# Kernel optimization log

Measured on AMD Instinct MI355X. Metric: run time of the kernel, lower is better.

The kernel has to match this reference:

```python
import jax, jax.numpy as jnp
import numpy as np

H = 128
K = 20
N = 100000
B = 65536
TIME_SCALE = 1.0
NEG = -1e9


def setup_inputs() -> dict:
    key = jax.random.key(0)
    ks = jax.random.split(key, 16)
    s = 0.05
    return {
        "edge_index": jax.random.randint(ks[0], (2, B), 0, N),
        "edge_timestamp": jax.random.randint(ks[1], (B,), 0, 1000000),
        "hist_neighbors": jax.random.randint(ks[2], (N, K), 0, N),
        "hist_times": jax.random.randint(ks[3], (N, K), 0, 1000000),
        "hist_signs": jax.random.randint(ks[4], (N, K), 0, 2),
        "node_emb": jax.random.normal(ks[5], (N, H), jnp.float32) * s,
        "sign_emb": jax.random.normal(ks[6], (2, H), jnp.float32) * s,
        "tp_w1": jax.random.normal(ks[7], (H,), jnp.float32) * s,   # Linear(1,H) weight (flattened)
        "tp_b1": jax.random.normal(ks[8], (H,), jnp.float32) * s,
        "tp_w2": jax.random.normal(ks[9], (H, H), jnp.float32) * s,  # stored [in,out]
        "tp_b2": jax.random.normal(ks[10], (H,), jnp.float32) * s,
        "em_w1": jax.random.normal(ks[11], (4 * H, H), jnp.float32) * s,
        "em_b1": jax.random.normal(ks[12], (H,), jnp.float32) * s,
        "em_w2": jax.random.normal(ks[13], (H, 1), jnp.float32) * s,
        "em_b2": jax.random.normal(ks[14], (1,), jnp.float32) * s,
    }


def _encode(node_ids, query_times, hist_neighbors, hist_times, hist_signs,
            node_emb, sign_emb, tp_w1, tp_b1, tp_w2, tp_b2):
    # node_ids, query_times: [B]
    neigh = hist_neighbors[node_ids]   # [B,K]
    times = hist_times[node_ids]       # [B,K]
    signs = hist_signs[node_ids]       # [B,K]
    valid = (neigh != -1) & (times < query_times[:, None])
    neigh_c = jnp.where(neigh == -1, 0, neigh)
    neigh_e = node_emb[neigh_c]        # [B,K,H]
    sign_e = sign_emb[signs]           # [B,K,H]
    delta = (query_times[:, None].astype(jnp.float32) - times.astype(jnp.float32)) / TIME_SCALE
    h = jax.nn.relu(delta[..., None] * tp_w1 + tp_b1)           # [B,K,H]
    time_e = jnp.einsum('bkh,hd->bkd', h, tp_w2) + tp_b2        # [B,K,H]
    keys = neigh_e + sign_e + time_e
    query = node_emb[node_ids][:, None]                          # [B,1,H]
    scores = jnp.sum(query * keys, axis=-1) / jnp.sqrt(jnp.float32(H))
    scores = jnp.where(valid, scores, NEG)
    attn = jax.nn.softmax(scores, axis=1)                        # [B,K]
    return jnp.einsum('bk,bkh->bh', attn, keys)                  # [B,H]


def reference(edge_index, edge_timestamp, hist_neighbors, hist_times, hist_signs,
              node_emb, sign_emb, tp_w1, tp_b1, tp_w2, tp_b2,
              em_w1, em_b1, em_w2, em_b2):
    u, v = edge_index[0], edge_index[1]
    zu = _encode(u, edge_timestamp, hist_neighbors, hist_times, hist_signs,
                 node_emb, sign_emb, tp_w1, tp_b1, tp_w2, tp_b2)
    zv = _encode(v, edge_timestamp, hist_neighbors, hist_times, hist_signs,
                 node_emb, sign_emb, tp_w1, tp_b1, tp_w2, tp_b2)
    feat = jnp.concatenate([zu, zv, jnp.abs(zu - zv), zu * zv], axis=1)  # [B,4H]
    hid = jax.nn.relu(feat @ em_w1 + em_b1)
    logits = (hid @ em_w2 + em_b2).squeeze(-1)                           # [B]
    return logits
```

## Files before the change

### kernel.cpp

```cpp
#include <hip/hip_runtime.h>
#include <hip/hip_bf16.h>
#include <math.h>

#define H 128
#define K 20
#define EPB 16

#define WS_TBL    0
#define WS_THM    65792
#define WS_CNT    66176
#define WSB_HI    67072
#define WSB_LO    99840

typedef __attribute__((ext_vector_type(8))) short short8;
typedef __attribute__((ext_vector_type(4))) float f32x4;

template<int CTRL, int RMASK>
__device__ __forceinline__ float dpp_add(float x) {
  int y = __builtin_amdgcn_update_dpp(0, __float_as_int(x), CTRL, RMASK, 0xf, true);
  return x + __int_as_float(y);
}
__device__ __forceinline__ float wave_sum63(float x) {
  x = dpp_add<0xB1,  0xf>(x);
  x = dpp_add<0x4E,  0xf>(x);
  x = dpp_add<0x141, 0xf>(x);
  x = dpp_add<0x140, 0xf>(x);
  x = dpp_add<0x142, 0xa>(x);
  x = dpp_add<0x143, 0xc>(x);
  return x;
}
__device__ __forceinline__ float bcast63(float x) {
  return __int_as_float(__builtin_amdgcn_readlane(__float_as_int(x), 63));
}

__device__ __forceinline__ unsigned short bfbits(float x) {
  __hip_bfloat16 h = __float2bfloat16(x);
  unsigned short u; __builtin_memcpy(&u, &h, 2); return u;
}
__device__ __forceinline__ float bf2f(unsigned short u) {
  return __uint_as_float(((unsigned)u) << 16);
}

__global__ __launch_bounds__(128) void aux_kernel(
    const float* __restrict__ w1v, const float* __restrict__ b1v,
    const float* __restrict__ w2, const float* __restrict__ b2,
    const float* __restrict__ em_w1, float* __restrict__ ws)
{
  int blk = blockIdx.x;
  int tid = threadIdx.x;
  if (blk < 257) {
    __shared__ float th[H];
    __shared__ int grp[H];
    __shared__ int sidx[2 * H];
    __shared__ int Msh;
    float w = w1v[tid], b = b1v[tid];
    int g = (w > 0.f) ? 0 : ((w < 0.f) ? 1 : 2);
    float t = (g == 2) ? 0.f : (-b / w);
    th[tid] = t; grp[tid] = g;
    if (tid == 0) Msh = 0;
    __syncthreads();
    if (g != 2) {
      int r = 0;
      for (int i = 0; i < H; i++)
        if (grp[i] != 2 && (th[i] < t || (th[i] == t && i < tid))) r++;
      sidx[r] = (tid << 1) | (g == 0 ? 1 : 0);
      atomicAdd(&Msh, 1);
      if (blk == 0) ws[WS_THM + r] = t;
    }
    __syncthreads();
    int M = Msh;
    if (blk == 0 && tid == 0) ((int*)(ws + WS_CNT))[0] = M;
    int r = blk;
    if (r > M) return;
    int d = tid;
    float accW = 0.f, accB = b2[d];
    for (int i = 0; i < H; i++)
      if (grp[i] == 2 && b1v[i] > 0.f) accB += b1v[i] * w2[i * H + d];
    #pragma unroll 4
    for (int i = 0; i < M; i++) {
      int ent = sidx[i];
      int h = ent >> 1;
      int isP = ent & 1;
      int take = (i < r) ? isP : (1 - isP);
      if (take) {
        float wv = w2[h * H + d];
        accW += w1v[h] * wv;
        accB += b1v[h] * wv;
      }
    }
    ws[WS_TBL + r * 256 + 2 * d + 0] = accW;
    ws[WS_TBL + r * 256 + 2 * d + 1] = accB;
  } else {
    int idx = (blk - 257) * 128 + tid;
    int j  = idx & 7;
    int l  = (idx >> 3) & 63;
    int kc = (idx >> 9) & 15;
    int c  = idx >> 13;
    int k = kc * 32 + ((l >> 4) * 8) + j;
    int n = c * 16 + (l & 15);
    float x = em_w1[k * H + n];
    unsigned short hb = bfbits(x);
    unsigned short lb = bfbits(x - bf2f(hb));
    ((unsigned short*)(ws + WSB_HI))[idx] = hb;
    ((unsigned short*)(ws + WSB_LO))[idx] = lb;
  }
}

template<int NB>
__device__ __forceinline__ void run_sides(
    int sbase, int b0, int B, int lane,
    const int* __restrict__ edge_index, const int* __restrict__ edge_ts,
    const int* __restrict__ hist_nb, const int* __restrict__ hist_tm,
    const int* __restrict__ hist_sg,
    const float* __restrict__ node_emb, const float* __restrict__ ws,
    float th0, float th1, float th2, float th3,
    float2 se0, float2 se1, float* __restrict__ zbuf)
{
  const float S = 0.088388347648318447f;
  int eBase = sbase >> 1;
  int eN = b0 + eBase;
  int nU = edge_index[eN];
  int nV = edge_index[B + eN];
  int t_n = edge_ts[eN];
  float2 qU_n = *(const float2*)(node_emb + (size_t)nU * H + 2 * lane);
  float2 qV_n = *(const float2*)(node_emb + (size_t)nV * H + 2 * lane);
  int pkU_n = 0, tmU_n = 0, pkV_n = 0, tmV_n = 0;
  if (lane < K) {
    pkU_n = (hist_nb[nU * K + lane] << 1) | hist_sg[nU * K + lane];
    tmU_n = hist_tm[nU * K + lane];
    pkV_n = (hist_nb[nV * K + lane] << 1) | hist_sg[nV * K + lane];
    tmV_n = hist_tm[nV * K + lane];
  }

  #pragma unroll 1
  for (int p = 0; p < 4; p++) {
    int e = eBase + p;
    int tC = t_n;
    float2 qU = qU_n, qV = qV_n;
    int pkU = pkU_n, tmU = tmU_n, pkV = pkV_n, tmV = tmV_n;
    if (p < 3) {
      int e2 = b0 + e + 1;
      int nU2 = edge_index[e2];
      int nV2 = edge_index[B + e2];
      t_n = edge_ts[e2];
      qU_n = *(const float2*)(node_emb + (size_t)nU2 * H + 2 * lane);
      qV_n = *(const float2*)(node_emb + (size_t)nV2 * H + 2 * lane);
      if (lane < K) {
        pkU_n = (hist_nb[nU2 * K + lane] << 1) | hist_sg[nU2 * K + lane];
        tmU_n = hist_tm[nU2 * K + lane];
        pkV_n = (hist_nb[nV2 * K + lane] << 1) | hist_sg[nV2 * K + lane];
        tmV_n = hist_tm[nV2 * K + lane];
      }
    }

    unsigned long long mU0 = __ballot((lane < K) && (tmU < tC) && (pkU >= 0));
    unsigned long long mV0 = __ballot((lane < K) && (tmV < tC) && (pkV >= 0));
    bool fU = (mU0 == 0), fV = (mV0 == 0);
    unsigned long long mU = fU ? 0xFFFFFull : mU0;
    unsigned long long mV = fV ? 0xFFFFFull : mV0;
    float qUx = qU.x * S, qUy = qU.y * S;
    float qVx = qV.x * S, qVy = qV.y * S;

    float mxU = -3.0e38f, ssU = 0.f, zU0 = 0.f, zU1 = 0.f;
    float mxV = -3.0e38f, ssV = 0.f, zV0 = 0.f, zV1 = 0.f;
    while (mU | mV) {
      bool vUa = mU != 0; int kUa = vUa ? (__ffsll((long long)mU) - 1) : 0; mU &= mU - 1;
      bool vUb = mU != 0; int kUb = vUb ? (__ffsll((long long)mU) - 1) : 0; mU &= mU - 1;
      bool vVa = mV != 0; int kVa = vVa ? (__ffsll((long long)mV) - 1) : 0; mV &= mV - 1;
      bool vVb = mV != 0; int kVb = vVb ? (__ffsll((long long)mV) - 1) : 0; mV &= mV - 1;

      int tmkUa = __builtin_amdgcn_readlane(tmU, kUa);
      int pkkUa = __builtin_amdgcn_readlane(pkU, kUa);
      int tmkUb = __builtin_amdgcn_readlane(tmU, kUb);
      int pkkUb = __builtin_amdgcn_readlane(pkU, kUb);
      int tmkVa = __builtin_amdgcn_readlane(tmV, kVa);
      int pkkVa = __builtin_amdgcn_readlane(pkV, kVa);
      int tmkVb = __builtin_amdgcn_readlane(tmV, kVb);
      int pkkVb = __builtin_amdgcn_readlane(pkV, kVb);

      float dUa = (float)tC - (float)tmkUa;
      float dUb = (float)tC - (float)tmkUb;
      float dVa = (float)tC - (float)tmkVa;
      float dVb = (float)tC - (float)tmkVb;

      int rUa = __popcll(__ballot(th0 < dUa)) + __popcll(__ballot(th1 < dUa));
      int rUb = __popcll(__ballot(th0 < dUb)) + __popcll(__ballot(th1 < dUb));
      int rVa = __popcll(__ballot(th0 < dVa)) + __popcll(__ballot(th1 < dVa));
      int rVb = __popcll(__ballot(th0 < dVb)) + __popcll(__ballot(th1 < dVb));
      if (NB == 4) {
        rUa += __popcll(__ballot(th2 < dUa)) + __popcll(__ballot(th3 < dUa));
        rUb += __popcll(__ballot(th2 < dUb)) + __popcll(__ballot(th3 < dUb));
        rVa += __popcll(__ballot(th2 < dVa)) + __popcll(__ballot(th3 < dVa));
        rVb += __popcll(__ballot(th2 < dVb)) + __popcll(__ballot(th3 < dVb));
      }

      const float4 tUa = *(const float4*)(ws + WS_TBL + rUa * 256 + 4 * lane);
      const float4 tUb = *(const float4*)(ws + WS_TBL + rUb * 256 + 4 * lane);
      const float4 tVa = *(const float4*)(ws + WS_TBL + rVa * 256 + 4 * lane);
      const float4 tVb = *(const float4*)(ws + WS_TBL + rVb * 256 + 4 * lane);
      int nUa = (pkkUa < 0) ? 0 : (pkkUa >> 1);
      int nUb = (pkkUb < 0) ? 0 : (pkkUb >> 1);
      int nVa = (pkkVa < 0) ? 0 : (pkkVa >> 1);
      int nVb = (pkkVb < 0) ? 0 : (pkkVb >> 1);
      float2 eUa = *(const float2*)(node_emb + (size_t)nUa * H + 2 * lane);
      float2 eUb = *(const float2*)(node_emb + (size_t)nUb * H + 2 * lane);
      float2 eVa = *(const float2*)(node_emb + (size_t)nVa * H + 2 * lane);
      float2 eVb = *(const float2*)(node_emb + (size_t)nVb * H + 2 * lane);

      float kUa0 = eUa.x + ((pkkUa & 1) ? se1.x : se0.x) + dUa * tUa.x + tUa.y;
      float kUa1 = eUa.y + ((pkkUa & 1) ? se1.y : se0.y) + dUa * tUa.z + tUa.w;
      float kUb0 = eUb.x + ((pkkUb & 1) ? se1.x : se0.x) + dUb * tUb.x + tUb.y;
      float kUb1 = eUb.y + ((pkkUb & 1) ? se1.y : se0.y) + dUb * tUb.z + tUb.w;
      float kVa0 = eVa.x + ((pkkVa & 1) ? se1.x : se0.x) + dVa * tVa.x + tVa.y;
      float kVa1 = eVa.y + ((pkkVa & 1) ? se1.y : se0.y) + dVa * tVa.z + tVa.w;
      float kVb0 = eVb.x + ((pkkVb & 1) ? se1.x : se0.x) + dVb * tVb.x + tVb.y;
      float kVb1 = eVb.y + ((pkkVb & 1) ? se1.y : se0.y) + dVb * tVb.z + tVb.w;

      float pUa = wave_sum63(qUx * kUa0 + qUy * kUa1);
      float pUb = wave_sum63(qUx * kUb0 + qUy * kUb1);
      float pVa = wave_sum63(qVx * kVa0 + qVy * kVa1);
      float pVb = wave_sum63(qVx * kVb0 + qVy * kVb1);

      float sUa = (vUa && !fU) ? bcast63(pUa) : -1e9f;
      float sUb = (vUb && !fU) ? bcast63(pUb) : -1e9f;
      float sVa = (vVa && !fV) ? bcast63(pVa) : -1e9f;
      float sVb = (vVb && !fV) ? bcast63(pVb) : -1e9f;

      float mnU = fmaxf(mxU, fmaxf(sUa, sUb));
      float alU = __expf(mxU - mnU);
      float paU = __expf(sUa - mnU);
      float pbU = __expf(sUb - mnU);
      ssU = ssU * alU + paU + pbU;
      zU0 = zU0 * alU + paU * kUa0 + pbU * kUb0;
      zU1 = zU1 * alU + paU * kUa1 + pbU * kUb1;
      mxU = mnU;

      float mnV = fmaxf(mxV, fmaxf(sVa, sVb));
      float alV = __expf(mxV - mnV);
      float paV = __expf(sVa - mnV);
      float pbV = __expf(sVb - mnV);
      ssV = ssV * alV + paV + pbV;
      zV0 = zV0 * alV + paV * kVa0 + pbV * kVb0;
      zV1 = zV1 * alV + paV * kVa1 + pbV * kVb1;
      mxV = mnV;
    }

    float invU = 1.f / ssU; zU0 *= invU; zU1 *= invU;
    float invV = 1.f / ssV; zV0 *= invV; zV1 *= invV;

    int sw = (e & 7) << 1;
    int ccU = lane ^ sw;
    int ccV = (64 + lane) ^ sw;
    *(float2*)&zbuf[(e << 8) + (ccU << 1)] = make_float2(zU0, zU1);
    *(float2*)&zbuf[(e << 8) + (ccV << 1)] = make_float2(zV0, zV1);
  }
}

__global__ __launch_bounds__(256, 4) void tgat_main_kernel(
    const int* __restrict__ edge_index, const int* __restrict__ edge_ts,
    const int* __restrict__ hist_nb, const int* __restrict__ hist_tm,
    const int* __restrict__ hist_sg,
    const float* __restrict__ node_emb, const float* __restrict__ sign_emb,
    const float* __restrict__ em_b1,
    const float* __restrict__ em_w2, const float* __restrict__ em_b2,
    const float* __restrict__ ws, float* __restrict__ out, int B)
{
  __shared__ __align__(16) float zbuf[EPB * 256];

  int tid = threadIdx.x;
  int lane = tid & 63;
  int wv = __builtin_amdgcn_readfirstlane(tid >> 6);
  int b0 = blockIdx.x * EPB;

  int M = ((const int*)(ws + WS_CNT))[0];
  float th0 = (lane       < M) ? ws[WS_THM + lane      ] : 3.0e38f;
  float th1 = (lane + 64  < M) ? ws[WS_THM + lane + 64 ] : 3.0e38f;
  float2 se0 = *(const float2*)(sign_emb + 2 * lane);
  float2 se1 = *(const float2*)(sign_emb + H + 2 * lane);

  int sbase = wv * 8;
  if (M <= 128) {
    run_sides<2>(sbase, b0, B, lane, edge_index, edge_ts, hist_nb, hist_tm,
                 hist_sg, node_emb, ws, th0, th1, 3.0e38f, 3.0e38f,
                 se0, se1, zbuf);
  } else {
    float th2 = (lane + 128 < M) ? ws[WS_THM + lane + 128] : 3.0e38f;
    float th3 = (lane + 192 < M) ? ws[WS_THM + lane + 192] : 3.0e38f;
    run_sides<4>(sbase, b0, B, lane, edge_index, edge_ts, hist_nb, hist_tm,
                 hist_sg, node_emb, ws, th0, th1, th2, th3,
                 se0, se1, zbuf);
  }
  __syncthreads();

  const unsigned short* whi = (const unsigned short*)(ws + WSB_HI);
  const unsigned short* wlo = (const unsigned short*)(ws + WSB_LO);
  int c0 = 2 * wv;
  int m_ = lane & 15;
  int qd = lane >> 4;
  int sw = (m_ & 7) << 1;
  const float* zrow = zbuf + (m_ << 8);
  f32x4 acc0 = {0.f, 0.f, 0.f, 0.f};
  f32x4 acc1 = {0.f, 0.f, 0.f, 0.f};
  #pragma unroll
  for (int kc = 0; kc < 16; kc++) {
    const int reg = kc >> 2;
    int cb = (kc & 3) * 16 + qd * 4;
    float av[8];
    if (reg == 0) {
      float4 A0 = *(const float4*)(zrow + (((cb    ) ^ sw) << 1));
      float4 A1 = *(const float4*)(zrow + (((cb + 2) ^ sw) << 1));
      av[0]=A0.x; av[1]=A0.y; av[2]=A0.z; av[3]=A0.w;
      av[4]=A1.x; av[5]=A1.y; av[6]=A1.z; av[7]=A1.w;
    } else if (reg == 1) {
      float4 A0 = *(const float4*)(zrow + (((cb + 64) ^ sw) << 1));
      float4 A1 = *(const float4*)(zrow + (((cb + 66) ^ sw) << 1));
      av[0]=A0.x; av[1]=A0.y; av[2]=A0.z; av[3]=A0.w;
      av[4]=A1.x; av[5]=A1.y; av[6]=A1.z; av[7]=A1.w;
    } else {
      float4 U0 = *(const float4*)(zrow + (((cb    ) ^ sw) << 1));
      float4 U1 = *(const float4*)(zrow + (((cb + 2) ^ sw) << 1));
      float4 V0 = *(const float4*)(zrow + (((cb + 64) ^ sw) << 1));
      float4 V1 = *(const float4*)(zrow + (((cb + 66) ^ sw) << 1));
      float uu[8] = {U0.x,U0.y,U0.z,U0.w,U1.x,U1.y,U1.z,U1.w};
      float vvv[8] = {V0.x,V0.y,V0.z,V0.w,V1.x,V1.y,V1.z,V1.w};
      if (reg == 2) {
        #pragma unroll
        for (int j = 0; j < 8; j++) av[j] = fabsf(uu[j] - vvv[j]);
      } else {
        #pragma unroll
        for (int j = 0; j < 8; j++) av[j] = uu[j] * vvv[j];
      }
    }
    union { short8 v; unsigned u[4]; } ahi, alo;
    #pragma unroll
    for (int j = 0; j < 4; j++) {
      unsigned b0u = __float_as_uint(av[2 * j]);
      unsigned b1u = __float_as_uint(av[2 * j + 1]);
      ahi.u[j] = __builtin_amdgcn_perm(b1u, b0u, 0x07060302u);
      float l0 = av[2 * j]     - __uint_as_float(b0u & 0xFFFF0000u);
      float l1 = av[2 * j + 1] - __uint_as_float(b1u & 0xFFFF0000u);
      __hip_bfloat162 lp = __float22bfloat162_rn(make_float2(l0, l1));
      __builtin_memcpy(&alo.u[j], &lp, 4);
    }
    int f0 = (((c0    ) * 16 + kc) * 64 + lane) * 8;
    int f1 = (((c0 + 1) * 16 + kc) * 64 + lane) * 8;
    short8 bh0 = *(const short8*)(whi + f0);
    short8 bl0 = *(const short8*)(wlo + f0);
    short8 bh1 = *(const short8*)(whi + f1);
    short8 bl1 = *(const short8*)(wlo + f1);
    acc0 = __builtin_amdgcn_mfma_f32_16x16x32_bf16(ahi.v, bh0, acc0, 0, 0, 0);
    acc0 = __builtin_amdgcn_mfma_f32_16x16x32_bf16(ahi.v, bl0, acc0, 0, 0, 0);
    acc0 = __builtin_amdgcn_mfma_f32_16x16x32_bf16(alo.v, bh0, acc0, 0, 0, 0);
    acc1 = __builtin_amdgcn_mfma_f32_16x16x32_bf16(ahi.v, bh1, acc1, 0, 0, 0);
    acc1 = __builtin_amdgcn_mfma_f32_16x16x32_bf16(ahi.v, bl1, acc1, 0, 0, 0);
    acc1 = __builtin_amdgcn_mfma_f32_16x16x32_bf16(alo.v, bh1, acc1, 0, 0, 0);
  }
  __syncthreads();

  float* hp = zbuf;
  float eb0 = em_b1[c0 * 16 + m_];
  float eb1 = em_b1[(c0 + 1) * 16 + m_];
  #pragma unroll
  for (int r = 0; r < 4; r++) {
    int edge = qd * 4 + r;
    hp[edge * 132 + c0 * 16 + m_]       = fmaxf(acc0[r] + eb0, 0.f);
    hp[edge * 132 + (c0 + 1) * 16 + m_] = fmaxf(acc1[r] + eb1, 0.f);
  }
  __syncthreads();

  float2 w2v = *(const float2*)(em_w2 + 2 * lane);
  float bias2 = em_b2[0];
  #pragma unroll
  for (int i = 0; i < 4; i++) {
    int e = wv * 4 + i;
    int b = b0 + e;
    float2 hv = *(const float2*)(hp + e * 132 + 2 * lane);
    float p = wave_sum63(hv.x * w2v.x + hv.y * w2v.y);
    float ps = bcast63(p);
    if (lane == 0 && b < B) out[b] = ps + bias2;
  }
}

extern "C" void kernel_launch(void* const* d_in, const int* in_sizes, int n_in,
                              void* d_out, int out_size, void* d_ws, size_t ws_size,
                              hipStream_t stream)
{
  (void)n_in; (void)out_size; (void)ws_size;
  const int* edge_index = (const int*)d_in[0];
  const int* edge_ts    = (const int*)d_in[1];
  const int* hist_nb    = (const int*)d_in[2];
  const int* hist_tm    = (const int*)d_in[3];
  const int* hist_sg    = (const int*)d_in[4];
  const float* node_emb = (const float*)d_in[5];
  const float* sign_emb = (const float*)d_in[6];
  const float* tp_w1    = (const float*)d_in[7];
  const float* tp_b1    = (const float*)d_in[8];
  const float* tp_w2    = (const float*)d_in[9];
  const float* tp_b2    = (const float*)d_in[10];
  const float* em_w1    = (const float*)d_in[11];
  const float* em_b1    = (const float*)d_in[12];
  const float* em_w2    = (const float*)d_in[13];
  const float* em_b2    = (const float*)d_in[14];
  float* out = (float*)d_out;
  float* ws  = (float*)d_ws;
  int B = in_sizes[1];

  hipLaunchKernelGGL(aux_kernel, dim3(769), dim3(128), 0, stream,
                     tp_w1, tp_b1, tp_w2, tp_b2, em_w1, ws);
  int grid = (B + EPB - 1) / EPB;
  hipLaunchKernelGGL(tgat_main_kernel, dim3(grid), dim3(256), 0, stream,
                     edge_index, edge_ts, hist_nb, hist_tm, hist_sg,
                     node_emb, sign_emb, em_b1, em_w2, em_b2, ws, out, B);
}
```

Measured before the change: 367.9 us.

## Software-pipeline neighbor gathers one pair ahead of online-softmax consume

```diff
diff --git a/kernel.cpp b/kernel.cpp
--- a/kernel.cpp
+++ b/kernel.cpp
@@ -106,6 +106,14 @@
   }
 }
 
+struct KPair {
+  float4 tU0, tU1, tV0, tV1;
+  float2 eU0, eU1, eV0, eV1;
+  float  dU0, dU1, dV0, dV1;
+  int    sU0, sU1, sV0, sV1;
+  bool   hU, aU1, hV, aV1;
+};
+
 template<int NB>
 __device__ __forceinline__ void run_sides(
     int sbase, int b0, int B, int lane,
@@ -163,86 +171,110 @@
 
     float mxU = -3.0e38f, ssU = 0.f, zU0 = 0.f, zU1 = 0.f;
     float mxV = -3.0e38f, ssV = 0.f, zV0 = 0.f, zV1 = 0.f;
-    while (mU | mV) {
-      bool vUa = mU != 0; int kUa = vUa ? (__ffsll((long long)mU) - 1) : 0; mU &= mU - 1;
-      bool vUb = mU != 0; int kUb = vUb ? (__ffsll((long long)mU) - 1) : 0; mU &= mU - 1;
-      bool vVa = mV != 0; int kVa = vVa ? (__ffsll((long long)mV) - 1) : 0; mV &= mV - 1;
-      bool vVb = mV != 0; int kVb = vVb ? (__ffsll((long long)mV) - 1) : 0; mV &= mV - 1;
-
-      int tmkUa = __builtin_amdgcn_readlane(tmU, kUa);
-      int pkkUa = __builtin_amdgcn_readlane(pkU, kUa);
-      int tmkUb = __builtin_amdgcn_readlane(tmU, kUb);
-      int pkkUb = __builtin_amdgcn_readlane(pkU, kUb);
-      int tmkVa = __builtin_amdgcn_readlane(tmV, kVa);
-      int pkkVa = __builtin_amdgcn_readlane(pkV, kVa);
-      int tmkVb = __builtin_amdgcn_readlane(tmV, kVb);
-      int pkkVb = __builtin_amdgcn_readlane(pkV, kVb);
-
-      float dUa = (float)tC - (float)tmkUa;
-      float dUb = (float)tC - (float)tmkUb;
-      float dVa = (float)tC - (float)tmkVa;
-      float dVb = (float)tC - (float)tmkVb;
-
-      int rUa = __popcll(__ballot(th0 < dUa)) + __popcll(__ballot(th1 < dUa));
-      int rUb = __popcll(__ballot(th0 < dUb)) + __popcll(__ballot(th1 < dUb));
-      int rVa = __popcll(__ballot(th0 < dVa)) + __popcll(__ballot(th1 < dVa));
-      int rVb = __popcll(__ballot(th0 < dVb)) + __popcll(__ballot(th1 < dVb));
-      if (NB == 4) {
-        rUa += __popcll(__ballot(th2 < dUa)) + __popcll(__ballot(th3 < dUa));
-        rUb += __popcll(__ballot(th2 < dUb)) + __popcll(__ballot(th3 < dUb));
-        rVa += __popcll(__ballot(th2 < dVa)) + __popcll(__ballot(th3 < dVa));
-        rVb += __popcll(__ballot(th2 < dVb)) + __popcll(__ballot(th3 < dVb));
-      }
-
-      const float4 tUa = *(const float4*)(ws + WS_TBL + rUa * 256 + 4 * lane);
-      const float4 tUb = *(const float4*)(ws + WS_TBL + rUb * 256 + 4 * lane);
-      const float4 tVa = *(const float4*)(ws + WS_TBL + rVa * 256 + 4 * lane);
-      const float4 tVb = *(const float4*)(ws + WS_TBL + rVb * 256 + 4 * lane);
-      int nUa = (pkkUa < 0) ? 0 : (pkkUa >> 1);
-      int nUb = (pkkUb < 0) ? 0 : (pkkUb >> 1);
-      int nVa = (pkkVa < 0) ? 0 : (pkkVa >> 1);
-      int nVb = (pkkVb < 0) ? 0 : (pkkVb >> 1);
-      float2 eUa = *(const float2*)(node_emb + (size_t)nUa * H + 2 * lane);
-      float2 eUb = *(const float2*)(node_emb + (size_t)nUb * H + 2 * lane);
-      float2 eVa = *(const float2*)(node_emb + (size_t)nVa * H + 2 * lane);
-      float2 eVb = *(const float2*)(node_emb + (size_t)nVb * H + 2 * lane);
-
-      float kUa0 = eUa.x + ((pkkUa & 1) ? se1.x : se0.x) + dUa * tUa.x + tUa.y;
-      float kUa1 = eUa.y + ((pkkUa & 1) ? se1.y : se0.y) + dUa * tUa.z + tUa.w;
-      float kUb0 = eUb.x + ((pkkUb & 1) ? se1.x : se0.x) + dUb * tUb.x + tUb.y;
-      float kUb1 = eUb.y + ((pkkUb & 1) ? se1.y : se0.y) + dUb * tUb.z + tUb.w;
-      float kVa0 = eVa.x + ((pkkVa & 1) ? se1.x : se0.x) + dVa * tVa.x + tVa.y;
-      float kVa1 = eVa.y + ((pkkVa & 1) ? se1.y : se0.y) + dVa * tVa.z + tVa.w;
-      float kVb0 = eVb.x + ((pkkVb & 1) ? se1.x : se0.x) + dVb * tVb.x + tVb.y;
-      float kVb1 = eVb.y + ((pkkVb & 1) ? se1.y : se0.y) + dVb * tVb.z + tVb.w;
-
-      float pUa = wave_sum63(qUx * kUa0 + qUy * kUa1);
-      float pUb = wave_sum63(qUx * kUb0 + qUy * kUb1);
-      float pVa = wave_sum63(qVx * kVa0 + qVy * kVa1);
-      float pVb = wave_sum63(qVx * kVb0 + qVy * kVb1);
-
-      float sUa = (vUa && !fU) ? bcast63(pUa) : -1e9f;
-      float sUb = (vUb && !fU) ? bcast63(pUb) : -1e9f;
-      float sVa = (vVa && !fV) ? bcast63(pVa) : -1e9f;
-      float sVb = (vVb && !fV) ? bcast63(pVb) : -1e9f;
-
-      float mnU = fmaxf(mxU, fmaxf(sUa, sUb));
-      float alU = __expf(mxU - mnU);
-      float paU = __expf(sUa - mnU);
-      float pbU = __expf(sUb - mnU);
-      ssU = ssU * alU + paU + pbU;
-      zU0 = zU0 * alU + paU * kUa0 + pbU * kUb0;
-      zU1 = zU1 * alU + paU * kUa1 + pbU * kUb1;
-      mxU = mnU;
-
-      float mnV = fmaxf(mxV, fmaxf(sVa, sVb));
-      float alV = __expf(mxV - mnV);
-      float paV = __expf(sVa - mnV);
-      float pbV = __expf(sVb - mnV);
-      ssV = ssV * alV + paV + pbV;
-      zV0 = zV0 * alV + paV * kVa0 + pbV * kVb0;
-      zV1 = zV1 * alV + paV * kVa1 + pbV * kVb1;
-      mxV = mnV;
+
+    auto stage = [&](KPair &P) {
+      P.hU = (mU != 0);
+      if (P.hU) {
+        int kA = __ffsll((long long)mU) - 1; mU &= mU - 1;
+        bool vB = (mU != 0);
+        int kB = vB ? (__ffsll((long long)mU) - 1) : kA; mU &= mU - 1;
+        P.aU1 = vB;
+        int tmA = __builtin_amdgcn_readlane(tmU, kA);
+        int pkA = __builtin_amdgcn_readlane(pkU, kA);
+        int tmB = __builtin_amdgcn_readlane(tmU, kB);
+        int pkB = __builtin_amdgcn_readlane(pkU, kB);
+        float dA = (float)(tC - tmA);
+        float dB = (float)(tC - tmB);
+        P.dU0 = dA; P.dU1 = dB;
+        P.sU0 = pkA & 1; P.sU1 = pkB & 1;
+        int rA = __popcll(__ballot(th0 < dA)) + __popcll(__ballot(th1 < dA));
+        int rB = __popcll(__ballot(th0 < dB)) + __popcll(__ballot(th1 < dB));
+        if (NB == 4) {
+          rA += __popcll(__ballot(th2 < dA)) + __popcll(__ballot(th3 < dA));
+          rB += __popcll(__ballot(th2 < dB)) + __popcll(__ballot(th3 < dB));
+        }
+        P.tU0 = *(const float4*)(ws + WS_TBL + rA * 256 + 4 * lane);
+        P.tU1 = *(const float4*)(ws + WS_TBL + rB * 256 + 4 * lane);
+        P.eU0 = *(const float2*)(node_emb + (size_t)(pkA >> 1) * H + 2 * lane);
+        P.eU1 = *(const float2*)(node_emb + (size_t)(pkB >> 1) * H + 2 * lane);
+      }
+      P.hV = (mV != 0);
+      if (P.hV) {
+        int kA = __ffsll((long long)mV) - 1; mV &= mV - 1;
+        bool vB = (mV != 0);
+        int kB = vB ? (__ffsll((long long)mV) - 1) : kA; mV &= mV - 1;
+        P.aV1 = vB;
+        int tmA = __builtin_amdgcn_readlane(tmV, kA);
+        int pkA = __builtin_amdgcn_readlane(pkV, kA);
+        int tmB = __builtin_amdgcn_readlane(tmV, kB);
+        int pkB = __builtin_amdgcn_readlane(pkV, kB);
+        float dA = (float)(tC - tmA);
+        float dB = (float)(tC - tmB);
+        P.dV0 = dA; P.dV1 = dB;
+        P.sV0 = pkA & 1; P.sV1 = pkB & 1;
+        int rA = __popcll(__ballot(th0 < dA)) + __popcll(__ballot(th1 < dA));
+        int rB = __popcll(__ballot(th0 < dB)) + __popcll(__ballot(th1 < dB));
+        if (NB == 4) {
+          rA += __popcll(__ballot(th2 < dA)) + __popcll(__ballot(th3 < dA));
+          rB += __popcll(__ballot(th2 < dB)) + __popcll(__ballot(th3 < dB));
+        }
+        P.tV0 = *(const float4*)(ws + WS_TBL + rA * 256 + 4 * lane);
+        P.tV1 = *(const float4*)(ws + WS_TBL + rB * 256 + 4 * lane);
+        P.eV0 = *(const float2*)(node_emb + (size_t)(pkA >> 1) * H + 2 * lane);
+        P.eV1 = *(const float2*)(node_emb + (size_t)(pkB >> 1) * H + 2 * lane);
+      }
+    };
+
+    auto consume = [&](const KPair &P) {
+      if (P.hU) {
+        float kA0 = P.eU0.x + (P.sU0 ? se1.x : se0.x) + P.dU0 * P.tU0.x + P.tU0.y;
+        float kA1 = P.eU0.y + (P.sU0 ? se1.y : se0.y) + P.dU0 * P.tU0.z + P.tU0.w;
+        float kB0 = P.eU1.x + (P.sU1 ? se1.x : se0.x) + P.dU1 * P.tU1.x + P.tU1.y;
+        float kB1 = P.eU1.y + (P.sU1 ? se1.y : se0.y) + P.dU1 * P.tU1.z + P.tU1.w;
+        float pA = wave_sum63(qUx * kA0 + qUy * kA1);
+        float pB = wave_sum63(qUx * kB0 + qUy * kB1);
+        float sA = fU ? -1e9f : bcast63(pA);
+        float sB = (P.aU1 && !fU) ? bcast63(pB) : (P.aU1 ? -1e9f : -3.0e38f);
+        float mn = fmaxf(mxU, fmaxf(sA, sB));
+        float al = __expf(mxU - mn);
+        float wA = __expf(sA - mn);
+        float wB = __expf(sB - mn);
+        ssU = ssU * al + wA + wB;
+        zU0 = zU0 * al + wA * kA0 + wB * kB0;
+        zU1 = zU1 * al + wA * kA1 + wB * kB1;
+        mxU = mn;
+      }
+      if (P.hV) {
+        float kA0 = P.eV0.x + (P.sV0 ? se1.x : se0.x) + P.dV0 * P.tV0.x + P.tV0.y;
+        float kA1 = P.eV0.y + (P.sV0 ? se1.y : se0.y) + P.dV0 * P.tV0.z + P.tV0.w;
+        float kB0 = P.eV1.x + (P.sV1 ? se1.x : se0.x) + P.dV1 * P.tV1.x + P.tV1.y;
+        float kB1 = P.eV1.y + (P.sV1 ? se1.y : se0.y) + P.dV1 * P.tV1.z + P.tV1.w;
+        float pA = wave_sum63(qVx * kA0 + qVy * kA1);
+        float pB = wave_sum63(qVx * kB0 + qVy * kB1);
+        float sA = fV ? -1e9f : bcast63(pA);
+        float sB = (P.aV1 && !fV) ? bcast63(pB) : (P.aV1 ? -1e9f : -3.0e38f);
+        float mn = fmaxf(mxV, fmaxf(sA, sB));
+        float al = __expf(mxV - mn);
+        float wA = __expf(sA - mn);
+        float wB = __expf(sB - mn);
+        ssV = ssV * al + wA + wB;
+        zV0 = zV0 * al + wA * kA0 + wB * kB0;
+        zV1 = zV1 * al + wA * kA1 + wB * kB1;
+        mxV = mn;
+      }
+    };
+
+    KPair PA, PB;
+    stage(PA);
+    for (;;) {
+      bool more = (mU | mV) != 0;
+      if (more) stage(PB);
+      consume(PA);
+      if (!more) break;
+      more = (mU | mV) != 0;
+      if (more) stage(PA);
+      consume(PB);
+      if (!more) break;
     }
 
     float invU = 1.f / ssU; zU0 *= invU; zU1 *= invU;
```

Result: slower. 388.6 us (+5.6%).
